# Optimization experiments

Hardware: AMD Instinct MI355X
Metric: run time of the kernel (lower is better)

The kernel has to match this reference:

```python
import jax, jax.numpy as jnp
import numpy as np

B, A, G, C = 16, 32768, 100, 81
OVERLAP_THRESH = 0.5
VAR0, VAR1 = 0.1, 0.2


def setup_inputs() -> dict:
    key = jax.random.key(0)
    ks = jax.random.split(key, 8)
    loc_pred = jax.random.normal(ks[0], (B, A, 2), jnp.float32) * 0.1
    conf_pred = jax.random.normal(ks[1], (B, A, C), jnp.float32)
    # anchors as 1D intervals [x0, x1] in [0, 1.1)
    a0 = jax.random.uniform(ks[2], (B, A), jnp.float32) * 0.9
    alen = 0.01 + 0.19 * jax.random.uniform(ks[3], (B, A), jnp.float32)
    refined_anchors = jnp.stack([a0, a0 + alen], axis=-1)
    # targets rows: [x0, x1, label]; label 0 marks padding / invalid GT
    g0 = jax.random.uniform(ks[4], (B, G), jnp.float32) * 0.8
    glen = 0.02 + 0.18 * jax.random.uniform(ks[5], (B, G), jnp.float32)
    labels = jax.random.randint(ks[6], (B, G), 1, C).astype(jnp.float32)
    labels = labels * (jnp.arange(G) < 80).astype(jnp.float32)  # last 20 GTs padded
    targets = jnp.stack([g0, g0 + glen, labels], axis=-1)
    ignore_flags = (jax.random.uniform(ks[7], (B, A), jnp.float32) < 0.1).astype(jnp.int32)
    return dict(loc_pred=loc_pred, conf_pred=conf_pred,
                refined_anchors=refined_anchors,
                ignore_flags_refined_anchor=ignore_flags,
                targets=targets)


def _match_one(targets, anchors, ignore):
    """SSD-style anchor<->GT matching for one image on 1D interval boxes.
    targets: [G,3], anchors: [A,2], ignore: [A] -> (loc_t [A,2], conf_t [A])."""
    boxes = targets[:, :2]            # [G,2]
    labels = targets[:, 2]            # [G]
    valid = labels > 0                # padding filter (cur_targets[:,-1] > 0)
    # 1D IoU matrix [G, A]
    inter = jnp.maximum(
        jnp.minimum(boxes[:, 1:2], anchors[None, :, 1])
        - jnp.maximum(boxes[:, 0:1], anchors[None, :, 0]), 0.0)
    len_g = boxes[:, 1] - boxes[:, 0]
    len_a = anchors[:, 1] - anchors[:, 0]
    iou = inter / (len_g[:, None] + len_a[None, :] - inter)
    iou = jnp.where(valid[:, None], iou, -1.0)  # invalid GTs never match

    best_truth_overlap = iou.max(axis=0)        # [A]
    best_truth_idx = iou.argmax(axis=0)         # [A]
    best_prior_idx = iou.argmax(axis=1)         # [G] best anchor per GT
    # force-match the best anchor of each valid GT (scatter; dropped for invalid)
    sc_idx = jnp.where(valid, best_prior_idx, A)
    best_truth_overlap = best_truth_overlap.at[sc_idx].set(2.0, mode='drop')
    best_truth_idx = best_truth_idx.at[sc_idx].set(jnp.arange(G), mode='drop')

    matched = boxes[best_truth_idx]             # [A,2]
    conf = labels[best_truth_idx].astype(jnp.int32)
    conf = jnp.where(best_truth_overlap < OVERLAP_THRESH, 0, conf)  # background
    conf = jnp.where(ignore > 0, -1, conf)      # ignored refined anchors

    # encode matched GT relative to anchor (center/size with variances)
    ac = (anchors[:, 0] + anchors[:, 1]) * 0.5
    asz = len_a
    gc = (matched[:, 0] + matched[:, 1]) * 0.5
    gsz = matched[:, 1] - matched[:, 0]
    loc = jnp.stack([(gc - ac) / (VAR0 * asz),
                     jnp.log(gsz / asz) / VAR1], axis=-1)
    return loc, conf


def reference(loc_pred, conf_pred, refined_anchors, ignore_flags_refined_anchor, targets):
    loc_t, conf_t = jax.vmap(_match_one)(targets, refined_anchors,
                                         ignore_flags_refined_anchor)
    pos = conf_t > 0                              # [B, A]
    # smooth L1 (beta=1), summed over positive anchors only
    d = loc_pred - loc_t
    ad = jnp.abs(d)
    sl1 = jnp.where(ad < 1.0, 0.5 * d * d, ad - 0.5)
    loss_l = jnp.sum(sl1 * pos[..., None].astype(sl1.dtype))
    total_num = jnp.sum(pos).astype(sl1.dtype)
    # Note: the hard-negative-mining sort on conf_pred is computed in the
    # original but its result never affects the returned loss_l.
    return loss_l / total_num
```

## Files before the change

kernel.cpp:

```cpp
#include <hip/hip_runtime.h>
#include <cstdint>

#define B_ 16
#define A_ 32768
#define G_ 100

constexpr int APB = 2048;
constexpr int K_  = APB / 256;

__global__ __launch_bounds__(256) void k_match(
    const float* __restrict__ anchors,
    const float* __restrict__ targets,
    unsigned long long* __restrict__ keys,
    float* __restrict__ bto,
    int* __restrict__ bti)
{
    __shared__ float sg0[G_], sg1[G_], slg[G_];
    __shared__ int   sva[G_];

    const int b     = blockIdx.y;
    const int chunk = blockIdx.x;
    const int tid   = threadIdx.x;

    if (tid < G_) {
        float t0 = targets[(b * G_ + tid) * 3 + 0];
        float t1 = targets[(b * G_ + tid) * 3 + 1];
        float lb = targets[(b * G_ + tid) * 3 + 2];
        sg0[tid] = t0;
        sg1[tid] = t1;
        slg[tid] = t1 - t0;
        sva[tid] = (lb > 0.0f) ? 1 : 0;
    }
    __syncthreads();

    const int base = chunk * APB;

    float a0[K_], a1[K_], la[K_];
#pragma unroll
    for (int k = 0; k < K_; ++k) {
        int a = base + tid + k * 256;
        float2 v = ((const float2*)anchors)[b * A_ + a];
        a0[k] = v.x;
        a1[k] = v.y;
        la[k] = v.y - v.x;
    }

    float bestV[K_];
    int   bestG[K_];
#pragma unroll
    for (int k = 0; k < K_; ++k) { bestV[k] = -2.0f; bestG[k] = 0; }

    for (int g = 0; g < G_; ++g) {
        const float g0 = sg0[g], g1 = sg1[g], lg = slg[g];
        const int valid = sva[g];

        float    gBest = -1.0f;
        unsigned gIdx  = 0;

#pragma unroll
        for (int k = 0; k < K_; ++k) {
            float inter = fminf(g1, a1[k]) - fmaxf(g0, a0[k]);
            inter = fmaxf(inter, 0.0f);
            float iou = inter / (lg + la[k] - inter);
            float val = valid ? iou : -1.0f;
            if (val > bestV[k]) { bestV[k] = val; bestG[k] = g; }
            if (iou > gBest) {
                gBest = iou;
                gIdx  = (unsigned)(base + tid + k * 256);
            }
        }

        if (valid) {
            unsigned long long key =
                ((unsigned long long)__float_as_uint(gBest) << 32) |
                (unsigned long long)(0xFFFFFFFFu - gIdx);
#pragma unroll
            for (int off = 32; off > 0; off >>= 1) {
                unsigned long long o = __shfl_xor(key, off, 64);
                if (o > key) key = o;
            }
            if ((tid & 63) == 0) atomicMax(&keys[b * G_ + g], key);
        }
    }

#pragma unroll
    for (int k = 0; k < K_; ++k) {
        int a = base + tid + k * 256;
        bto[b * A_ + a] = bestV[k];
        bti[b * A_ + a] = bestG[k];
    }
}

__global__ void k_scatter(
    const float* __restrict__ targets,
    const unsigned long long* __restrict__ keys,
    float* __restrict__ bto,
    int* __restrict__ bti)
{
    int b = threadIdx.x;
    if (b >= B_) return;
    for (int g = 0; g < G_; ++g) {
        float lb = targets[(b * G_ + g) * 3 + 2];
        if (lb > 0.0f) {
            unsigned aidx = 0xFFFFFFFFu -
                (unsigned)(keys[b * G_ + g] & 0xFFFFFFFFull);
            bto[b * A_ + aidx] = 2.0f;
            bti[b * A_ + aidx] = g;
        }
    }
}

__global__ __launch_bounds__(256) void k_loss(
    const float* __restrict__ loc_pred,
    const float* __restrict__ anchors,
    const int*   __restrict__ ignore,
    const float* __restrict__ targets,
    const float* __restrict__ bto,
    const int*   __restrict__ bti,
    float* __restrict__ accum)
{
    const int i = blockIdx.x * 256 + threadIdx.x;
    const int b = i / A_;

    float mysum = 0.0f, mycnt = 0.0f;

    float ov  = bto[i];
    int   g   = bti[i];
    int   ign = ignore[i];
    float lb  = targets[(b * G_ + g) * 3 + 2];

    bool pos = (ign == 0) && !(ov < 0.5f) && (lb > 0.0f);
    if (pos) {
        float m0 = targets[(b * G_ + g) * 3 + 0];
        float m1 = targets[(b * G_ + g) * 3 + 1];
        float2 av = ((const float2*)anchors)[i];
        float ac  = (av.x + av.y) * 0.5f;
        float asz = av.y - av.x;
        float gc  = (m0 + m1) * 0.5f;
        float gsz = m1 - m0;
        float lt0 = (gc - ac) / (0.1f * asz);
        float lt1 = logf(gsz / asz) / 0.2f;

        float2 lp = ((const float2*)loc_pred)[i];
        float d0 = lp.x - lt0, d1 = lp.y - lt1;
        float ad0 = fabsf(d0), ad1 = fabsf(d1);
        mysum = (ad0 < 1.0f ? 0.5f * d0 * d0 : ad0 - 0.5f) +
                (ad1 < 1.0f ? 0.5f * d1 * d1 : ad1 - 0.5f);
        mycnt = 1.0f;
    }

#pragma unroll
    for (int off = 32; off > 0; off >>= 1) {
        mysum += __shfl_down(mysum, off, 64);
        mycnt += __shfl_down(mycnt, off, 64);
    }
    __shared__ float ssum[4], scnt[4];
    int wid = threadIdx.x >> 6, lane = threadIdx.x & 63;
    if (lane == 0) { ssum[wid] = mysum; scnt[wid] = mycnt; }
    __syncthreads();
    if (threadIdx.x == 0) {
        float s = ssum[0] + ssum[1] + ssum[2] + ssum[3];
        float c = scnt[0] + scnt[1] + scnt[2] + scnt[3];
        if (s != 0.0f || c != 0.0f) {
            atomicAdd(&accum[0], s);
            atomicAdd(&accum[1], c);
        }
    }
}

__global__ void k_final(const float* __restrict__ accum, float* __restrict__ out)
{
    out[0] = accum[0] / accum[1];
}

extern "C" void kernel_launch(void* const* d_in, const int* in_sizes, int n_in,
                              void* d_out, int out_size, void* d_ws, size_t ws_size,
                              hipStream_t stream) {
    const float* loc_pred = (const float*)d_in[0];
    const float* anchors  = (const float*)d_in[2];
    const int*   ignore   = (const int*)d_in[3];
    const float* targets  = (const float*)d_in[4];
    float*       out      = (float*)d_out;

    char* ws = (char*)d_ws;
    unsigned long long* keys = (unsigned long long*)ws;
    float* accum = (float*)(ws + 12800);
    float* bto   = (float*)(ws + 16384);
    int*   bti   = (int*)(ws + 16384 + (size_t)B_ * A_ * 4);

    hipMemsetAsync(ws, 0, 16384, stream);

    dim3 g1(A_ / APB, B_);
    k_match<<<g1, 256, 0, stream>>>(anchors, targets, keys, bto, bti);
    k_scatter<<<1, 64, 0, stream>>>(targets, keys, bto, bti);
    k_loss<<<(B_ * A_) / 256, 256, 0, stream>>>(loc_pred, anchors, ignore,
                                                targets, bto, bti, accum);
    k_final<<<1, 1, 0, stream>>>(accum, out);
}
```

Measured before the change: 374.1 us.

## Split matching into per-anchor and per-GT kernels, replace serial scatter with forced map

Splits the fused matching kernel in two. One kernel does the per-anchor best-GT search over smaller chunks, giving more blocks, skipping invalid GTs and using a fast reciprocal. A separate grid of one block per (GT, image) does the per-GT best-anchor search and writes a forced-match map with atomicMax. This replaces the single-thread serial scatter kernel and the per-GT wave reductions that sat inside the hot loop. The loss kernel applies the forced map, which costs an extra 2 MB memset and read, and the approximate reciprocal may change argmax tie-breaking.

New measurement: 311.9 us. -16.6%, faster.

```diff
diff --git a/kernel.cpp b/kernel.cpp
--- a/kernel.cpp
+++ b/kernel.cpp
@@ -5,108 +5,104 @@
 #define A_ 32768
 #define G_ 100
 
-constexpr int APB = 2048;
-constexpr int K_  = APB / 256;
+constexpr int APBG = 512;
+constexpr int KG   = APBG / 256;
 
-__global__ __launch_bounds__(256) void k_match(
+__global__ __launch_bounds__(256) void k_best_g(
     const float* __restrict__ anchors,
     const float* __restrict__ targets,
-    unsigned long long* __restrict__ keys,
     float* __restrict__ bto,
     int* __restrict__ bti)
 {
-    __shared__ float sg0[G_], sg1[G_], slg[G_];
-    __shared__ int   sva[G_];
+    __shared__ float4 sg[G_];
 
-    const int b     = blockIdx.y;
-    const int chunk = blockIdx.x;
-    const int tid   = threadIdx.x;
+    const int b   = blockIdx.y;
+    const int tid = threadIdx.x;
 
     if (tid < G_) {
         float t0 = targets[(b * G_ + tid) * 3 + 0];
         float t1 = targets[(b * G_ + tid) * 3 + 1];
         float lb = targets[(b * G_ + tid) * 3 + 2];
-        sg0[tid] = t0;
-        sg1[tid] = t1;
-        slg[tid] = t1 - t0;
-        sva[tid] = (lb > 0.0f) ? 1 : 0;
+        sg[tid] = make_float4(t0, t1, t1 - t0, lb);
     }
     __syncthreads();
 
-    const int base = chunk * APB;
+    const int base = blockIdx.x * APBG;
 
-    float a0[K_], a1[K_], la[K_];
+    float a0[KG], a1[KG], la[KG], bi[KG], bu[KG], bv[KG];
+    int   bg[KG];
 #pragma unroll
-    for (int k = 0; k < K_; ++k) {
-        int a = base + tid + k * 256;
-        float2 v = ((const float2*)anchors)[b * A_ + a];
-        a0[k] = v.x;
-        a1[k] = v.y;
-        la[k] = v.y - v.x;
+    for (int k = 0; k < KG; ++k) {
+        float2 v = ((const float2*)anchors)[b * A_ + base + tid + k * 256];
+        a0[k] = v.x; a1[k] = v.y; la[k] = v.y - v.x;
+        bi[k] = -1.0f; bu[k] = 1.0f; bv[k] = -1.0f; bg[k] = 0;
     }
 
-    float bestV[K_];
-    int   bestG[K_];
+    for (int g = 0; g < G_; ++g) {
+        float4 t = sg[g];
+        if (!(t.w > 0.0f)) continue;
 #pragma unroll
-    for (int k = 0; k < K_; ++k) { bestV[k] = -2.0f; bestG[k] = 0; }
-
-    for (int g = 0; g < G_; ++g) {
-        const float g0 = sg0[g], g1 = sg1[g], lg = slg[g];
-        const int valid = sva[g];
-
-        float    gBest = -1.0f;
-        unsigned gIdx  = 0;
-
-#pragma unroll
-        for (int k = 0; k < K_; ++k) {
-            float inter = fminf(g1, a1[k]) - fmaxf(g0, a0[k]);
-            inter = fmaxf(inter, 0.0f);
-            float iou = inter / (lg + la[k] - inter);
-            float val = valid ? iou : -1.0f;
-            if (val > bestV[k]) { bestV[k] = val; bestG[k] = g; }
-            if (iou > gBest) {
-                gBest = iou;
-                gIdx  = (unsigned)(base + tid + k * 256);
-            }
-        }
-
-        if (valid) {
-            unsigned long long key =
-                ((unsigned long long)__float_as_uint(gBest) << 32) |
-                (unsigned long long)(0xFFFFFFFFu - gIdx);
-#pragma unroll
-            for (int off = 32; off > 0; off >>= 1) {
-                unsigned long long o = __shfl_xor(key, off, 64);
-                if (o > key) key = o;
-            }
-            if ((tid & 63) == 0) atomicMax(&keys[b * G_ + g], key);
+        for (int k = 0; k < KG; ++k) {
+            float inter = fmaxf(fminf(t.y, a1[k]) - fmaxf(t.x, a0[k]), 0.0f);
+            float u     = (t.z + la[k]) - inter;
+            float iou   = inter * __builtin_amdgcn_rcpf(u);
+            if (iou > bv[k]) { bv[k] = iou; bi[k] = inter; bu[k] = u; bg[k] = g; }
         }
     }
 
 #pragma unroll
-    for (int k = 0; k < K_; ++k) {
+    for (int k = 0; k < KG; ++k) {
         int a = base + tid + k * 256;
-        bto[b * A_ + a] = bestV[k];
-        bti[b * A_ + a] = bestG[k];
+        bto[b * A_ + a] = bi[k] / bu[k];
+        bti[b * A_ + a] = bg[k];
     }
 }
 
-__global__ void k_scatter(
+__global__ __launch_bounds__(256) void k_best_a(
+    const float* __restrict__ anchors,
     const float* __restrict__ targets,
-    const unsigned long long* __restrict__ keys,
-    float* __restrict__ bto,
-    int* __restrict__ bti)
+    int* __restrict__ forced)
 {
-    int b = threadIdx.x;
-    if (b >= B_) return;
-    for (int g = 0; g < G_; ++g) {
-        float lb = targets[(b * G_ + g) * 3 + 2];
-        if (lb > 0.0f) {
-            unsigned aidx = 0xFFFFFFFFu -
-                (unsigned)(keys[b * G_ + g] & 0xFFFFFFFFull);
-            bto[b * A_ + aidx] = 2.0f;
-            bti[b * A_ + aidx] = g;
-        }
+    const int g = blockIdx.x, b = blockIdx.y, tid = threadIdx.x;
+
+    float t0 = targets[(b * G_ + g) * 3 + 0];
+    float t1 = targets[(b * G_ + g) * 3 + 1];
+    float lb = targets[(b * G_ + g) * 3 + 2];
+    if (!(lb > 0.0f)) return;
+    float lg = t1 - t0;
+
+    float    bestV = -1.0f;
+    unsigned bestA = 0;
+    const float2* ap = (const float2*)anchors + b * A_;
+
+#pragma unroll 4
+    for (int j = 0; j < A_ / 256; ++j) {
+        int a = tid + j * 256;
+        float2 v = ap[a];
+        float la    = v.y - v.x;
+        float inter = fmaxf(fminf(t1, v.y) - fmaxf(t0, v.x), 0.0f);
+        float u     = (lg + la) - inter;
+        float iou   = inter * __builtin_amdgcn_rcpf(u);
+        if (iou > bestV) { bestV = iou; bestA = (unsigned)a; }
+    }
+
+    unsigned long long key =
+        ((unsigned long long)__float_as_uint(bestV) << 32) |
+        (unsigned long long)(0xFFFFFFFFu - bestA);
+#pragma unroll
+    for (int off = 32; off > 0; off >>= 1) {
+        unsigned long long o = __shfl_xor(key, off, 64);
+        if (o > key) key = o;
+    }
+    __shared__ unsigned long long sk[4];
+    if ((tid & 63) == 0) sk[tid >> 6] = key;
+    __syncthreads();
+    if (tid == 0) {
+        unsigned long long k0 = sk[0];
+#pragma unroll
+        for (int w = 1; w < 4; ++w) if (sk[w] > k0) k0 = sk[w];
+        unsigned aidx = 0xFFFFFFFFu - (unsigned)(k0 & 0xFFFFFFFFull);
+        atomicMax(&forced[b * A_ + aidx], g);
     }
 }
 
@@ -117,19 +113,21 @@
     const float* __restrict__ targets,
     const float* __restrict__ bto,
     const int*   __restrict__ bti,
+    const int*   __restrict__ forced,
     float* __restrict__ accum)
 {
     const int i = blockIdx.x * 256 + threadIdx.x;
-    const int b = i / A_;
+    const int b = i >> 15;
 
-    float mysum = 0.0f, mycnt = 0.0f;
-
-    float ov  = bto[i];
-    int   g   = bti[i];
+    float ov = bto[i];
+    int   g  = bti[i];
+    int   f  = forced[i];
+    if (f >= 0) { g = f; ov = 2.0f; }
     int   ign = ignore[i];
     float lb  = targets[(b * G_ + g) * 3 + 2];
 
-    bool pos = (ign == 0) && !(ov < 0.5f) && (lb > 0.0f);
+    float mysum = 0.0f, mycnt = 0.0f;
+    bool pos = (ign == 0) && (ov >= 0.5f) && (lb > 0.0f);
     if (pos) {
         float m0 = targets[(b * G_ + g) * 3 + 0];
         float m1 = targets[(b * G_ + g) * 3 + 1];
@@ -183,17 +181,19 @@
     float*       out      = (float*)d_out;
 
     char* ws = (char*)d_ws;
-    unsigned long long* keys = (unsigned long long*)ws;
-    float* accum = (float*)(ws + 12800);
-    float* bto   = (float*)(ws + 16384);
-    int*   bti   = (int*)(ws + 16384 + (size_t)B_ * A_ * 4);
+    float* accum  = (float*)ws;
+    int*   forced = (int*)(ws + 4096);
+    float* bto    = (float*)(ws + 4096 + (size_t)B_ * A_ * 4);
+    int*   bti    = (int*)(ws + 4096 + (size_t)B_ * A_ * 8);
 
-    hipMemsetAsync(ws, 0, 16384, stream);
+    hipMemsetAsync(accum, 0, 16, stream);
+    hipMemsetAsync(forced, 0xFF, (size_t)B_ * A_ * 4, stream);
 
-    dim3 g1(A_ / APB, B_);
-    k_match<<<g1, 256, 0, stream>>>(anchors, targets, keys, bto, bti);
-    k_scatter<<<1, 64, 0, stream>>>(targets, keys, bto, bti);
+    dim3 gg(A_ / APBG, B_);
+    k_best_g<<<gg, 256, 0, stream>>>(anchors, targets, bto, bti);
+    dim3 ga(G_, B_);
+    k_best_a<<<ga, 256, 0, stream>>>(anchors, targets, forced);
     k_loss<<<(B_ * A_) / 256, 256, 0, stream>>>(loc_pred, anchors, ignore,
-                                                targets, bto, bti, accum);
+                                                targets, bto, bti, forced, accum);
     k_final<<<1, 1, 0, stream>>>(accum, out);
 }
```
